# Kernel optimization log

Hardware: AMD Instinct MI355X
Metric: run time of the kernel (lower is better)

Reference implementation:

```python
import jax, jax.numpy as jnp
import numpy as np

B, N, DEG, H, NH, R = 8, 256, 32, 768, 12, 64


def setup_inputs() -> dict:
    key = jax.random.key(0)
    ks = jax.random.split(key, 8)
    node_states = jax.random.normal(ks[0], (B, N, H), dtype=jnp.float32)
    # deterministic unique neighbor sets, sorted per (b, src) so COO is coalesced
    i_row = np.arange(N)[:, None]                      # (N,1)
    j_row = np.sort((i_row + 1 + 7 * np.arange(DEG)[None, :]) % N, axis=1)  # (N,DEG)
    b_idx = np.repeat(np.arange(B), N * DEG)
    i_idx = np.tile(np.repeat(np.arange(N), DEG), B)
    j_idx = np.tile(j_row.reshape(-1), B)
    E = B * N * DEG
    r_idx = np.asarray(jax.random.randint(ks[1], (E,), 0, R))
    edge_indices = jnp.asarray(np.stack([b_idx, i_idx, j_idx, r_idx]), dtype=jnp.int32)
    s = 0.02
    Wq = s * jax.random.normal(ks[2], (H, H), dtype=jnp.float32)
    Wk = s * jax.random.normal(ks[3], (H, H), dtype=jnp.float32)
    Wv = s * jax.random.normal(ks[4], (H, H), dtype=jnp.float32)
    bq = jnp.zeros((H,), jnp.float32)
    bk = jnp.zeros((H,), jnp.float32)
    bv = jnp.zeros((H,), jnp.float32)
    Ek = s * jax.random.normal(ks[5], (R, H), dtype=jnp.float32)
    Ev = s * jax.random.normal(ks[6], (R, H), dtype=jnp.float32)
    Ek = Ek.at[0].set(0.0)  # TOKEN_TO_TOKEN relation embedding zeroed at init
    Ev = Ev.at[0].set(0.0)
    return {"node_states": node_states, "edge_indices": edge_indices,
            "Wq": Wq, "bq": bq, "Wk": Wk, "bk": bk, "Wv": Wv, "bv": bv,
            "Ek": Ek, "Ev": Ev, "num_heads": NH}


def reference(node_states, edge_indices, Wq, bq, Wk, bk, Wv, bv, Ek, Ev, num_heads):
    Bz, Nn, Hh = node_states.shape
    nh = num_heads
    dh = Hh // nh
    b, i, j, r = edge_indices[0], edge_indices[1], edge_indices[2], edge_indices[3]
    E = b.shape[0]
    # dense projections (compute once per node)
    Q = node_states @ Wq + bq
    Kn = node_states @ Wk + bk
    Vn = node_states @ Wv + bv
    # gather per edge, split heads: (E, nh, dh)
    Qe = Q[b, i].reshape(E, nh, dh)
    Kne = Kn[b, j].reshape(E, nh, dh)
    Kee = Ek[r].reshape(E, nh, dh)
    scale = 1.0 / jnp.sqrt(jnp.asarray(dh, node_states.dtype))
    # logits = (q.k_node + q.k_edge) / sqrt(dh) per head -> (E, nh)
    logits = (jnp.sum(Qe * Kne, -1) + jnp.sum(Qe * Kee, -1)) * scale
    # sparse softmax over target-node dim: segments = (batch, src) pairs
    seg = b * Nn + i
    nseg = Bz * Nn
    m = jax.ops.segment_max(logits, seg, num_segments=nseg)
    ex = jnp.exp(logits - m[seg])
    z = jax.ops.segment_sum(ex, seg, num_segments=nseg)
    attn = ex / z[seg]  # (E, nh); dropout prob = 0 (eval)
    # values: V_node[tgt] + V_edge  -> (E, nh, dh)
    Ve = (Vn[b, j] + Ev[r]).reshape(E, nh, dh)
    contrib = (attn[..., None] * Ve).reshape(E, Hh)
    out = jax.ops.segment_sum(contrib, seg, num_segments=nseg)
    return out.reshape(Bz, Nn, Hh)
```

## Files before the change

kernel.cpp:

```cpp
#include <hip/hip_runtime.h>
#include <hip/hip_bf16.h>
#include <cstdint>
#include <cstddef>

#define B_   8
#define N_   256
#define DEG_ 32
#define H_   768
#define NH_  12
#define E_   (B_*N_*DEG_)
#define M_   (B_*N_)

typedef __attribute__((ext_vector_type(8))) short short8;
typedef __attribute__((ext_vector_type(4))) float float4v;

static __device__ __forceinline__ short f2bf(float f) {
    __hip_bfloat16 h = __float2bfloat16(f);
    return *(short*)&h;
}

__global__ __launch_bounds__(256)
void cast_wt(const float* __restrict__ W0, const float* __restrict__ W1,
             const float* __restrict__ W2, short* __restrict__ Wt)
{
    const float* W = (blockIdx.z == 0) ? W0 : (blockIdx.z == 1) ? W1 : W2;
    short* Wo = Wt + (size_t)blockIdx.z * H_ * H_;
    __shared__ short tile[64][65];
    const int kb = blockIdx.y * 64, nb = blockIdx.x * 64;
    const int t = threadIdx.x;
    {
        const int k = t >> 2, nq = (t & 3) * 16;
        const float* src = W + (size_t)(kb + k) * H_ + nb + nq;
        #pragma unroll
        for (int q = 0; q < 16; q += 4) {
            const float4 v = *(const float4*)(src + q);
            tile[k][nq + q + 0] = f2bf(v.x);
            tile[k][nq + q + 1] = f2bf(v.y);
            tile[k][nq + q + 2] = f2bf(v.z);
            tile[k][nq + q + 3] = f2bf(v.w);
        }
    }
    __syncthreads();
    {
        const int n = t >> 2, kq = (t & 3) * 16;
        short8 o0, o1;
        #pragma unroll
        for (int j = 0; j < 8; ++j) o0[j] = tile[kq + j][n];
        #pragma unroll
        for (int j = 0; j < 8; ++j) o1[j] = tile[kq + 8 + j][n];
        short* dst = Wo + (size_t)(nb + n) * H_ + kb + kq;
        *(short8*)dst = o0;
        *(short8*)(dst + 8) = o1;
    }
}

#define BK 32
#define XP 40
#define WP 40

__global__ __launch_bounds__(256, 4)
void qkv_mfma(const float* __restrict__ X, const short* __restrict__ Wt,
              const float* __restrict__ bq, const float* __restrict__ bk,
              const float* __restrict__ bv,
              float* __restrict__ Qo, float* __restrict__ Ko, float* __restrict__ Vo)
{
    __shared__ __align__(16) short Xs[64 * XP];
    __shared__ __align__(16) short Ws[64 * WP];
    const int t = threadIdx.x;

    const int L    = blockIdx.x;
    const int xcd  = L & 7, slot = L >> 3;
    const int by   = xcd * 4 + (slot & 3);
    const int bx   = slot >> 2;
    const int mt   = bx / 12;
    const int n0   = (bx % 12) * 64;
    const int m0   = by * 64;
    const short* Wm = Wt + (size_t)mt * H_ * H_;

    const int wave = t >> 6, lane = t & 63;
    const int wr = wave >> 1, wc = wave & 1;
    const int quad = lane >> 4, lr = lane & 15;

    float4v acc[2][2];
    #pragma unroll
    for (int i = 0; i < 2; ++i)
        #pragma unroll
        for (int j = 0; j < 2; ++j)
            acc[i][j] = (float4v){0.f, 0.f, 0.f, 0.f};

    const int xrow = t >> 2, xk = (t & 3) * 8;
    const int wn   = t >> 2, wk = (t & 3) * 8;

    for (int kt = 0; kt < H_; kt += BK) {
        {
            const float* src = X + (size_t)(m0 + xrow) * H_ + kt + xk;
            const float4 a = *(const float4*)src;
            const float4 b = *(const float4*)(src + 4);
            short8 o;
            o[0] = f2bf(a.x); o[1] = f2bf(a.y); o[2] = f2bf(a.z); o[3] = f2bf(a.w);
            o[4] = f2bf(b.x); o[5] = f2bf(b.y); o[6] = f2bf(b.z); o[7] = f2bf(b.w);
            *(short8*)&Xs[xrow * XP + xk] = o;
        }
        {
            const short8 v = *(const short8*)(Wm + (size_t)(n0 + wn) * H_ + kt + wk);
            *(short8*)&Ws[wn * WP + wk] = v;
        }
        __syncthreads();

        short8 af[2], bf[2];
        #pragma unroll
        for (int i = 0; i < 2; ++i)
            af[i] = *(const short8*)&Xs[(wr * 32 + i * 16 + lr) * XP + quad * 8];
        #pragma unroll
        for (int j = 0; j < 2; ++j)
            bf[j] = *(const short8*)&Ws[(wc * 32 + j * 16 + lr) * WP + quad * 8];

        #pragma unroll
        for (int i = 0; i < 2; ++i)
            #pragma unroll
            for (int j = 0; j < 2; ++j)
                acc[i][j] = __builtin_amdgcn_mfma_f32_16x16x32_bf16(
                    af[i], bf[j], acc[i][j], 0, 0, 0);
        __syncthreads();
    }

    const float* bp = (mt == 0) ? bq : (mt == 1) ? bk : bv;
    float*       op = (mt == 0) ? Qo : (mt == 1) ? Ko : Vo;
    #pragma unroll
    for (int i = 0; i < 2; ++i) {
        #pragma unroll
        for (int j = 0; j < 2; ++j) {
            const int col = n0 + wc * 32 + j * 16 + lr;
            const float bias = bp[col];
            #pragma unroll
            for (int r4 = 0; r4 < 4; ++r4) {
                const int row = m0 + wr * 32 + i * 16 + quad * 4 + r4;
                op[(size_t)row * H_ + col] = acc[i][j][r4] + bias;
            }
        }
    }
}

__global__ __launch_bounds__(256)
void edge_attn(const float* __restrict__ Qm, const float* __restrict__ Km,
               const float* __restrict__ Vm, const int* __restrict__ eidx,
               const float* __restrict__ Ek, const float* __restrict__ Ev,
               float* __restrict__ out)
{
    __shared__ __align__(16) float qs[H_];
    __shared__ int   jj[DEG_];
    __shared__ int   rr[DEG_];
    __shared__ float lg[DEG_][13];

    const int bid = blockIdx.x;
    const int seg = ((bid & 7) << 8) | (bid >> 3);
    const int b   = seg >> 8;
    const int t   = threadIdx.x;
    const int e0  = seg * DEG_;

    if (t < 192) {
        ((float4*)qs)[t] = ((const float4*)(Qm + (size_t)seg * H_))[t];
    } else if (t < 224) {
        jj[t - 192] = eidx[2 * E_ + e0 + (t - 192)];
    } else {
        rr[t - 224] = eidx[3 * E_ + e0 + (t - 224)];
    }
    __syncthreads();

    const int wave = t >> 6, lane = t & 63;
    const int sub = lane >> 4, l16 = lane & 15;
    const size_t bN = (size_t)b * N_;

    float4 q4[NH_];
    #pragma unroll
    for (int h = 0; h < NH_; ++h)
        q4[h] = *(const float4*)&qs[h * 64 + l16 * 4];

    const float scale = 0.125f;
    #pragma unroll
    for (int it = 0; it < 2; ++it) {
        const int e = it * 16 + wave * 4 + sub;
        const int j = jj[e], r = rr[e];
        const float* kr = Km + (bN + j) * H_ + l16 * 4;
        const float* er = Ek + (size_t)r * H_ + l16 * 4;
        float p[NH_];
        #pragma unroll
        for (int h = 0; h < NH_; ++h) {
            const float4 kv = *(const float4*)(kr + h * 64);
            const float4 ev = *(const float4*)(er + h * 64);
            p[h] = q4[h].x * (kv.x + ev.x) + q4[h].y * (kv.y + ev.y)
                 + q4[h].z * (kv.z + ev.z) + q4[h].w * (kv.w + ev.w);
        }
        #pragma unroll
        for (int off = 8; off >= 1; off >>= 1)
            #pragma unroll
            for (int h = 0; h < NH_; ++h)
                p[h] += __shfl_xor(p[h], off);
        if (l16 == 0) {
            #pragma unroll
            for (int h = 0; h < NH_; ++h) lg[e][h] = p[h] * scale;
        }
    }
    __syncthreads();

    if (t < 192) {
        const int h = t >> 4, l = t & 15;
        const float a = lg[l][h], c = lg[l + 16][h];
        float m = fmaxf(a, c);
        #pragma unroll
        for (int off = 8; off >= 1; off >>= 1) m = fmaxf(m, __shfl_xor(m, off));
        const float ea = __expf(a - m), ec = __expf(c - m);
        float z = ea + ec;
        #pragma unroll
        for (int off = 8; off >= 1; off >>= 1) z += __shfl_xor(z, off);
        const float inv = 1.f / z;
        lg[l][h] = ea * inv;
        lg[l + 16][h] = ec * inv;
    }
    __syncthreads();

    if (t < 192) {
        const int h = t >> 4;
        const float* vbase  = Vm + bN * H_ + 4 * t;
        const float* evbase = Ev + 4 * t;
        float4 acc = {0.f, 0.f, 0.f, 0.f};
        #pragma unroll 4
        for (int e = 0; e < DEG_; ++e) {
            const float a = lg[e][h];
            const float4 v  = *(const float4*)(vbase  + (size_t)jj[e] * H_);
            const float4 ev = *(const float4*)(evbase + (size_t)rr[e] * H_);
            acc.x += a * (v.x + ev.x);
            acc.y += a * (v.y + ev.y);
            acc.z += a * (v.z + ev.z);
            acc.w += a * (v.w + ev.w);
        }
        *(float4*)(out + (size_t)seg * H_ + 4 * t) = acc;
    }
}

extern "C" void kernel_launch(void* const* d_in, const int* in_sizes, int n_in,
                              void* d_out, int out_size, void* d_ws, size_t ws_size,
                              hipStream_t stream)
{
    const float* X    = (const float*)d_in[0];
    const int*   eidx = (const int*)  d_in[1];
    const float* Wq   = (const float*)d_in[2];
    const float* bq   = (const float*)d_in[3];
    const float* Wk   = (const float*)d_in[4];
    const float* bk   = (const float*)d_in[5];
    const float* Wv   = (const float*)d_in[6];
    const float* bv   = (const float*)d_in[7];
    const float* Ek   = (const float*)d_in[8];
    const float* Ev   = (const float*)d_in[9];
    float* out = (float*)d_out;

    float* Q  = (float*)d_ws;
    float* K  = Q + (size_t)M_ * H_;
    float* V  = K + (size_t)M_ * H_;
    short* Wt = (short*)(V + (size_t)M_ * H_);

    cast_wt<<<dim3(H_ / 64, H_ / 64, 3), dim3(256), 0, stream>>>(Wq, Wk, Wv, Wt);
    qkv_mfma<<<dim3(1152), dim3(256), 0, stream>>>(X, Wt, bq, bk, bv, Q, K, V);
    edge_attn<<<dim3(M_), dim3(256), 0, stream>>>(Q, K, V, eidx, Ek, Ev, out);
}
```

Baseline: 134.1 us.

## Store Q/K/V and edge embeddings in bf16, pre-cast X, retile QKV GEMM

Adds a flat cast kernel that converts X, Ek and Ev to bf16 ahead of time. The QKV GEMM now reads bf16 X, uses 128x64 tiles with a K-step of 64, and writes bf16 Q/K/V. The edge attention kernel gathers bf16 K/V/Ek/Ev, halving the bytes of the scattered gathers, and now assigns 8 lanes per edge for the logits. The cost is lower precision in the intermediates, one extra launch, and the removal of the XCD-aware block remapping.

```diff
diff --git a/kernel.cpp b/kernel.cpp
--- a/kernel.cpp
+++ b/kernel.cpp
@@ -17,6 +17,28 @@
 static __device__ __forceinline__ short f2bf(float f) {
     __hip_bfloat16 h = __float2bfloat16(f);
     return *(short*)&h;
+}
+static __device__ __forceinline__ float bf2f(short s) {
+    return __uint_as_float(((unsigned)(unsigned short)s) << 16);
+}
+
+__global__ __launch_bounds__(256)
+void cast_flat(const float* __restrict__ X, const float* __restrict__ Ek,
+               const float* __restrict__ Ev, short* __restrict__ Xb,
+               short* __restrict__ Ekb, short* __restrict__ Evb)
+{
+    const int bid = blockIdx.x;
+    const float* src; short* dst; int base;
+    if (bid < 768)      { src = X;  dst = Xb;  base = bid * 2048; }
+    else if (bid < 792) { src = Ek; dst = Ekb; base = (bid - 768) * 2048; }
+    else                { src = Ev; dst = Evb; base = (bid - 792) * 2048; }
+    const int i = base + threadIdx.x * 8;
+    const float4 a = *(const float4*)(src + i);
+    const float4 b = *(const float4*)(src + i + 4);
+    short8 o;
+    o[0] = f2bf(a.x); o[1] = f2bf(a.y); o[2] = f2bf(a.z); o[3] = f2bf(a.w);
+    o[4] = f2bf(b.x); o[5] = f2bf(b.y); o[6] = f2bf(b.z); o[7] = f2bf(b.w);
+    *(short8*)(dst + i) = o;
 }
 
 __global__ __launch_bounds__(256)
@@ -54,97 +76,92 @@
     }
 }
 
-#define BK 32
-#define XP 40
-#define WP 40
-
-__global__ __launch_bounds__(256, 4)
-void qkv_mfma(const float* __restrict__ X, const short* __restrict__ Wt,
+#define XPITCH 68
+#define WPITCH 68
+
+__global__ __launch_bounds__(256, 2)
+void qkv_mfma(const short* __restrict__ Xb, const short* __restrict__ Wt,
               const float* __restrict__ bq, const float* __restrict__ bk,
               const float* __restrict__ bv,
-              float* __restrict__ Qo, float* __restrict__ Ko, float* __restrict__ Vo)
-{
-    __shared__ __align__(16) short Xs[64 * XP];
-    __shared__ __align__(16) short Ws[64 * WP];
+              short* __restrict__ Qo, short* __restrict__ Ko, short* __restrict__ Vo)
+{
+    __shared__ __align__(16) short Xs[128 * XPITCH];
+    __shared__ __align__(16) short Ws[64 * WPITCH];
     const int t = threadIdx.x;
-
-    const int L    = blockIdx.x;
-    const int xcd  = L & 7, slot = L >> 3;
-    const int by   = xcd * 4 + (slot & 3);
-    const int bx   = slot >> 2;
-    const int mt   = bx / 12;
-    const int n0   = (bx % 12) * 64;
-    const int m0   = by * 64;
+    const int mt = blockIdx.x / 12;
+    const int n0 = (blockIdx.x % 12) * 64;
+    const int m0 = blockIdx.y * 128;
     const short* Wm = Wt + (size_t)mt * H_ * H_;
 
     const int wave = t >> 6, lane = t & 63;
-    const int wr = wave >> 1, wc = wave & 1;
     const int quad = lane >> 4, lr = lane & 15;
 
-    float4v acc[2][2];
+    float4v acc[2][4];
     #pragma unroll
     for (int i = 0; i < 2; ++i)
         #pragma unroll
-        for (int j = 0; j < 2; ++j)
+        for (int j = 0; j < 4; ++j)
             acc[i][j] = (float4v){0.f, 0.f, 0.f, 0.f};
 
-    const int xrow = t >> 2, xk = (t & 3) * 8;
-    const int wn   = t >> 2, wk = (t & 3) * 8;
-
-    for (int kt = 0; kt < H_; kt += BK) {
+    const int xrow = t >> 1, xoff = (t & 1) * 8;
+    const int wrow = t >> 2, woff = (t & 3) * 16;
+
+    for (int kt = 0; kt < H_; kt += 64) {
         {
-            const float* src = X + (size_t)(m0 + xrow) * H_ + kt + xk;
-            const float4 a = *(const float4*)src;
-            const float4 b = *(const float4*)(src + 4);
-            short8 o;
-            o[0] = f2bf(a.x); o[1] = f2bf(a.y); o[2] = f2bf(a.z); o[3] = f2bf(a.w);
-            o[4] = f2bf(b.x); o[5] = f2bf(b.y); o[6] = f2bf(b.z); o[7] = f2bf(b.w);
-            *(short8*)&Xs[xrow * XP + xk] = o;
+            const short* src = Xb + (size_t)(m0 + xrow) * H_ + kt + xoff;
+            short* dst = &Xs[xrow * XPITCH + xoff];
+            #pragma unroll
+            for (int i = 0; i < 4; ++i)
+                *(short8*)(dst + i * 16) = *(const short8*)(src + i * 16);
         }
         {
-            const short8 v = *(const short8*)(Wm + (size_t)(n0 + wn) * H_ + kt + wk);
-            *(short8*)&Ws[wn * WP + wk] = v;
+            const short* src = Wm + (size_t)(n0 + wrow) * H_ + kt + woff;
+            short* dst = &Ws[wrow * WPITCH + woff];
+            *(short8*)dst = *(const short8*)src;
+            *(short8*)(dst + 8) = *(const short8*)(src + 8);
         }
         __syncthreads();
 
-        short8 af[2], bf[2];
-        #pragma unroll
-        for (int i = 0; i < 2; ++i)
-            af[i] = *(const short8*)&Xs[(wr * 32 + i * 16 + lr) * XP + quad * 8];
-        #pragma unroll
-        for (int j = 0; j < 2; ++j)
-            bf[j] = *(const short8*)&Ws[(wc * 32 + j * 16 + lr) * WP + quad * 8];
-
-        #pragma unroll
-        for (int i = 0; i < 2; ++i)
-            #pragma unroll
-            for (int j = 0; j < 2; ++j)
-                acc[i][j] = __builtin_amdgcn_mfma_f32_16x16x32_bf16(
-                    af[i], bf[j], acc[i][j], 0, 0, 0);
+        #pragma unroll
+        for (int kk = 0; kk < 2; ++kk) {
+            short8 af[2], bf[4];
+            #pragma unroll
+            for (int i = 0; i < 2; ++i)
+                af[i] = *(const short8*)&Xs[(wave * 32 + i * 16 + lr) * XPITCH + kk * 32 + quad * 8];
+            #pragma unroll
+            for (int j = 0; j < 4; ++j)
+                bf[j] = *(const short8*)&Ws[(j * 16 + lr) * WPITCH + kk * 32 + quad * 8];
+            #pragma unroll
+            for (int i = 0; i < 2; ++i)
+                #pragma unroll
+                for (int j = 0; j < 4; ++j)
+                    acc[i][j] = __builtin_amdgcn_mfma_f32_16x16x32_bf16(
+                        af[i], bf[j], acc[i][j], 0, 0, 0);
+        }
         __syncthreads();
     }
 
     const float* bp = (mt == 0) ? bq : (mt == 1) ? bk : bv;
-    float*       op = (mt == 0) ? Qo : (mt == 1) ? Ko : Vo;
+    short*       op = (mt == 0) ? Qo : (mt == 1) ? Ko : Vo;
     #pragma unroll
-    for (int i = 0; i < 2; ++i) {
-        #pragma unroll
-        for (int j = 0; j < 2; ++j) {
-            const int col = n0 + wc * 32 + j * 16 + lr;
-            const float bias = bp[col];
-            #pragma unroll
-            for (int r4 = 0; r4 < 4; ++r4) {
-                const int row = m0 + wr * 32 + i * 16 + quad * 4 + r4;
-                op[(size_t)row * H_ + col] = acc[i][j][r4] + bias;
+    for (int j = 0; j < 4; ++j) {
+        const int col = n0 + j * 16 + lr;
+        const float bias = bp[col];
+        #pragma unroll
+        for (int i = 0; i < 2; ++i) {
+            #pragma unroll
+            for (int r = 0; r < 4; ++r) {
+                const int row = m0 + wave * 32 + i * 16 + quad * 4 + r;
+                op[(size_t)row * H_ + col] = f2bf(acc[i][j][r] + bias);
             }
         }
     }
 }
 
 __global__ __launch_bounds__(256)
-void edge_attn(const float* __restrict__ Qm, const float* __restrict__ Km,
-               const float* __restrict__ Vm, const int* __restrict__ eidx,
-               const float* __restrict__ Ek, const float* __restrict__ Ev,
+void edge_attn(const short* __restrict__ Qm, const short* __restrict__ Km,
+               const short* __restrict__ Vm, const int* __restrict__ eidx,
+               const short* __restrict__ Ekb, const short* __restrict__ Evb,
                float* __restrict__ out)
 {
     __shared__ __align__(16) float qs[H_];
@@ -159,7 +176,11 @@
     const int e0  = seg * DEG_;
 
     if (t < 192) {
-        ((float4*)qs)[t] = ((const float4*)(Qm + (size_t)seg * H_))[t];
+        const short4 q = *(const short4*)(Qm + (size_t)seg * H_ + t * 4);
+        qs[t * 4 + 0] = bf2f(q.x);
+        qs[t * 4 + 1] = bf2f(q.y);
+        qs[t * 4 + 2] = bf2f(q.z);
+        qs[t * 4 + 3] = bf2f(q.w);
     } else if (t < 224) {
         jj[t - 192] = eidx[2 * E_ + e0 + (t - 192)];
     } else {
@@ -168,37 +189,40 @@
     __syncthreads();
 
     const int wave = t >> 6, lane = t & 63;
-    const int sub = lane >> 4, l16 = lane & 15;
+    const int e    = wave * 8 + (lane >> 3);
+    const int l8   = lane & 7;
     const size_t bN = (size_t)b * N_;
 
-    float4 q4[NH_];
-    #pragma unroll
-    for (int h = 0; h < NH_; ++h)
-        q4[h] = *(const float4*)&qs[h * 64 + l16 * 4];
-
-    const float scale = 0.125f;
-    #pragma unroll
-    for (int it = 0; it < 2; ++it) {
-        const int e = it * 16 + wave * 4 + sub;
+    {
         const int j = jj[e], r = rr[e];
-        const float* kr = Km + (bN + j) * H_ + l16 * 4;
-        const float* er = Ek + (size_t)r * H_ + l16 * 4;
+        const short* kr = Km  + (bN + j) * H_ + l8 * 8;
+        const short* er = Ekb + (size_t)r * H_ + l8 * 8;
         float p[NH_];
         #pragma unroll
         for (int h = 0; h < NH_; ++h) {
-            const float4 kv = *(const float4*)(kr + h * 64);
-            const float4 ev = *(const float4*)(er + h * 64);
-            p[h] = q4[h].x * (kv.x + ev.x) + q4[h].y * (kv.y + ev.y)
-                 + q4[h].z * (kv.z + ev.z) + q4[h].w * (kv.w + ev.w);
-        }
-        #pragma unroll
-        for (int off = 8; off >= 1; off >>= 1)
+            const float4 qa = *(const float4*)&qs[h * 64 + l8 * 8];
+            const float4 qb = *(const float4*)&qs[h * 64 + l8 * 8 + 4];
+            const short8 kv = *(const short8*)(kr + h * 64);
+            const short8 ev = *(const short8*)(er + h * 64);
+            float s;
+            s  = qa.x * (bf2f(kv[0]) + bf2f(ev[0]));
+            s += qa.y * (bf2f(kv[1]) + bf2f(ev[1]));
+            s += qa.z * (bf2f(kv[2]) + bf2f(ev[2]));
+            s += qa.w * (bf2f(kv[3]) + bf2f(ev[3]));
+            s += qb.x * (bf2f(kv[4]) + bf2f(ev[4]));
+            s += qb.y * (bf2f(kv[5]) + bf2f(ev[5]));
+            s += qb.z * (bf2f(kv[6]) + bf2f(ev[6]));
+            s += qb.w * (bf2f(kv[7]) + bf2f(ev[7]));
+            p[h] = s;
+        }
+        #pragma unroll
+        for (int off = 4; off >= 1; off >>= 1)
             #pragma unroll
             for (int h = 0; h < NH_; ++h)
                 p[h] += __shfl_xor(p[h], off);
-        if (l16 == 0) {
-            #pragma unroll
-            for (int h = 0; h < NH_; ++h) lg[e][h] = p[h] * scale;
+        if (l8 == 0) {
+            #pragma unroll
+            for (int h = 0; h < NH_; ++h) lg[e][h] = p[h] * 0.125f;
         }
     }
     __syncthreads();
@@ -221,18 +245,18 @@
 
     if (t < 192) {
         const int h = t >> 4;
-        const float* vbase  = Vm + bN * H_ + 4 * t;
-        const float* evbase = Ev + 4 * t;
+        const short* vbase  = Vm + bN * H_ + 4 * t;
+        const short* evbase = Evb + 4 * t;
         float4 acc = {0.f, 0.f, 0.f, 0.f};
         #pragma unroll 4
-        for (int e = 0; e < DEG_; ++e) {
-            const float a = lg[e][h];
-            const float4 v  = *(const float4*)(vbase  + (size_t)jj[e] * H_);
-            const float4 ev = *(const float4*)(evbase + (size_t)rr[e] * H_);
-            acc.x += a * (v.x + ev.x);
-            acc.y += a * (v.y + ev.y);
-            acc.z += a * (v.z + ev.z);
-            acc.w += a * (v.w + ev.w);
+        for (int e2 = 0; e2 < DEG_; ++e2) {
+            const float a = lg[e2][h];
+            const short4 v  = *(const short4*)(vbase  + (size_t)jj[e2] * H_);
+            const short4 ev = *(const short4*)(evbase + (size_t)rr[e2] * H_);
+            acc.x += a * (bf2f(v.x) + bf2f(ev.x));
+            acc.y += a * (bf2f(v.y) + bf2f(ev.y));
+            acc.z += a * (bf2f(v.z) + bf2f(ev.z));
+            acc.w += a * (bf2f(v.w) + bf2f(ev.w));
         }
         *(float4*)(out + (size_t)seg * H_ + 4 * t) = acc;
     }
@@ -254,12 +278,16 @@
     const float* Ev   = (const float*)d_in[9];
     float* out = (float*)d_out;
 
-    float* Q  = (float*)d_ws;
-    float* K  = Q + (size_t)M_ * H_;
-    float* V  = K + (size_t)M_ * H_;
-    short* Wt = (short*)(V + (size_t)M_ * H_);
-
+    short* Qb  = (short*)d_ws;
+    short* Kb  = Qb + (size_t)M_ * H_;
+    short* Vb  = Kb + (size_t)M_ * H_;
+    short* Xb  = Vb + (size_t)M_ * H_;
+    short* Wt  = Xb + (size_t)M_ * H_;
+    short* Ekb = Wt + (size_t)3 * H_ * H_;
+    short* Evb = Ekb + (size_t)64 * H_;
+
+    cast_flat<<<dim3(816), dim3(256), 0, stream>>>(X, Ek, Ev, Xb, Ekb, Evb);
     cast_wt<<<dim3(H_ / 64, H_ / 64, 3), dim3(256), 0, stream>>>(Wq, Wk, Wv, Wt);
-    qkv_mfma<<<dim3(1152), dim3(256), 0, stream>>>(X, Wt, bq, bk, bv, Q, K, V);
-    edge_attn<<<dim3(M_), dim3(256), 0, stream>>>(Q, K, V, eidx, Ek, Ev, out);
-}
+    qkv_mfma<<<dim3(36, 16), dim3(256), 0, stream>>>(Xb, Wt, bq, bk, bv, Qb, Kb, Vb);
+    edge_attn<<<dim3(M_), dim3(256), 0, stream>>>(Qb, Kb, Vb, eidx, Ekb, Evb, out);
+}
```

Measured after the change: 143.7 us. 1.07x slower.
